# Performance work log

Hardware: AMD Instinct MI355X
Metric: run time of the kernel (lower is better)

The kernel has to match this reference:

```python
import jax, jax.numpy as jnp
import numpy as np

S, B, H = 2048, 32, 1024

def setup_inputs() -> dict:
    key = jax.random.key(0)
    ks = jax.random.split(key, 8)
    return {
        "hidden": jax.random.normal(ks[0], (1, B, H), dtype=jnp.float32),
        "hidden_sequence": jax.random.normal(ks[1], (S, B, H), dtype=jnp.float32),
        "input_masks": jax.random.bernoulli(ks[2], 0.5, (S, B)),
        "W1": jax.random.normal(ks[3], (H, H), dtype=jnp.float32) * 0.02,
        "b1": jax.random.normal(ks[4], (H,), dtype=jnp.float32) * 0.02,
        "W2": jax.random.normal(ks[5], (H, H), dtype=jnp.float32) * 0.02,
        "b2": jax.random.normal(ks[6], (H,), dtype=jnp.float32) * 0.02,
        "v": jax.random.uniform(ks[7], (H,), dtype=jnp.float32),
    }

def reference(hidden, hidden_sequence, input_masks, W1, b1, W2, b2, v):
    # hidden: (1,B,H) broadcast over S; hidden_sequence: (S,B,H)
    # additive (Bahdanau) energy: v . tanh(W1 hs + W2 h)  -> (S,B)
    pre = (jnp.einsum('sbh,kh->sbk', hidden_sequence, W1) + b1
           + jnp.einsum('obh,kh->obk', hidden, W2) + b2)  # (S,B,H)
    energy = jnp.einsum('sbh,h->sb', jnp.tanh(pre), v)     # (S,B)
    energy = jnp.where(input_masks, energy, jnp.float32(-1e10))
    attn = jax.nn.softmax(energy, axis=0)                  # softmax over seq per batch
    context = jnp.einsum('sb,sbh->bh', attn, hidden_sequence)[None]  # (1,B,H)
    return context
```

## Files before the change

### kernel.cpp

```cpp
#include <hip/hip_runtime.h>
#include <stdint.h>


#define SS 2048
#define BB 32
#define HH 1024
#define MM (SS*BB)

typedef _Float16 f16;
typedef __attribute__((ext_vector_type(8))) _Float16 f16x8;
typedef __attribute__((ext_vector_type(4))) _Float16 f16x4;
typedef __attribute__((ext_vector_type(4))) float   floatx4;

__device__ __forceinline__ float tanh_fast(float x) {
  float e = __expf(2.0f * x);
  return 1.0f - 2.0f / (e + 1.0f);
}

__device__ __forceinline__ void gload16(void* lds_base, const void* gptr) {
  __builtin_amdgcn_global_load_lds(
      (const __attribute__((address_space(1))) uint32_t*)(uintptr_t)gptr,
      (__attribute__((address_space(3))) uint32_t*)(uint32_t)(uintptr_t)lds_base,
      16, 0, 0);
}

#define BAR()   __builtin_amdgcn_s_barrier()
#define LGKM0() asm volatile("s_waitcnt lgkmcnt(0)" ::: "memory")
#define VMC4()  asm volatile("s_waitcnt vmcnt(4)" ::: "memory")
#define VMC0()  asm volatile("s_waitcnt vmcnt(0)" ::: "memory")

__global__ __launch_bounds__(256) void convert_f16(
    const float* __restrict__ hs, const float* __restrict__ W1,
    f16* __restrict__ hsf, f16* __restrict__ W1f)
{
  const size_t NH = (size_t)MM * HH;
  size_t base = ((size_t)blockIdx.x * 256 + threadIdx.x) * 8;
  if (base < NH) {
    floatx4 a = *(const floatx4*)&hs[base];
    floatx4 b = *(const floatx4*)&hs[base + 4];
    f16x8 o = {(f16)a.x,(f16)a.y,(f16)a.z,(f16)a.w,(f16)b.x,(f16)b.y,(f16)b.z,(f16)b.w};
    *(f16x8*)&hsf[base] = o;
  } else {
    size_t wb = base - NH;
    if (wb < (size_t)HH * HH) {
      floatx4 a = *(const floatx4*)&W1[wb];
      floatx4 b = *(const floatx4*)&W1[wb + 4];
      f16x8 o = {(f16)a.x,(f16)a.y,(f16)a.z,(f16)a.w,(f16)b.x,(f16)b.y,(f16)b.z,(f16)b.w};
      *(f16x8*)&W1f[wb] = o;
    }
  }
}

__global__ __launch_bounds__(256) void t2_kernel(
    const float* __restrict__ hidden, const float* __restrict__ W2,
    const float* __restrict__ b1, const float* __restrict__ b2,
    float* __restrict__ t2)
{
  const int gw   = blockIdx.x * 4 + (threadIdx.x >> 6);
  const int n    = gw >> 5;
  const int b    = gw & 31;
  const int lane = threadIdx.x & 63;
  float acc = 0.f;
#pragma unroll
  for (int q = 0; q < 4; ++q) {
    floatx4 hv = *(const floatx4*)&hidden[b * HH + q * 256 + lane * 4];
    floatx4 wv = *(const floatx4*)&W2[(size_t)n * HH + q * 256 + lane * 4];
    acc += hv.x * wv.x + hv.y * wv.y + hv.z * wv.z + hv.w * wv.w;
  }
#pragma unroll
  for (int off = 1; off < 64; off <<= 1) acc += __shfl_xor(acc, off);
  if (lane == 0) t2[b * HH + n] = acc + b1[n] + b2[n];
}

__global__ __launch_bounds__(512, 2) void gemm_energy_8p(
    const f16* __restrict__ hsf, const f16* __restrict__ W1f,
    const float* __restrict__ t2, const float* __restrict__ v,
    float* __restrict__ epart)
{
  __shared__ __align__(16) f16 Asm[2][2][128 * 64];
  __shared__ __align__(16) f16 Bsm[2][2][128 * 64];

  const int tid  = threadIdx.x;
  const int lane = tid & 63;
  const int w    = tid >> 6;
  const int quad = lane >> 4;
  const int l15  = lane & 15;
  const int wr   = w >> 2;
  const int wc   = w & 3;

  const int l  = blockIdx.x;
  const int x  = l & 7;
  const int j_ = l >> 3;
  const int nb = j_ & 3;
  const int mt = (j_ >> 2) * 8 + x;
  const int mB = mt * 256;
  const int nB = nb * 256;

  const int srow = w * 8 + (lane >> 3);
  const int sc0  = lane & 7;

  auto stA = [&](int buf, int half, int kt) {
#pragma unroll
    for (int q = 0; q < 2; ++q) {
      const int r  = q * 64 + srow;
      const int cb = sc0 ^ (r & 7);
      gload16(&Asm[buf][half][(q * 64 + w * 8) * 64],
              &hsf[(size_t)(mB + half * 128 + r) * HH + kt + cb * 8]);
    }
  };
  auto stB = [&](int buf, int half, int kt) {
#pragma unroll
    for (int q = 0; q < 2; ++q) {
      const int r  = q * 64 + srow;
      const int cb = sc0 ^ (r & 7);
      gload16(&Bsm[buf][half][(q * 64 + w * 8) * 64],
              &W1f[(size_t)(nB + half * 128 + r) * HH + kt + cb * 8]);
    }
  };

  floatx4 acc[8][4];
#pragma unroll
  for (int i = 0; i < 8; ++i)
#pragma unroll
    for (int j = 0; j < 4; ++j) acc[i][j] = (floatx4){0.f, 0.f, 0.f, 0.f};

  stB(0, 0, 0); stA(0, 0, 0); stA(0, 1, 0); stB(0, 1, 0);
  stB(1, 0, 64); stA(1, 0, 64);
  VMC4();
  BAR();

  f16x8 aF[2][4], b0F[2][2], b1F[2][2];
  const int bhalf  = wc >> 1;
  const int brbase = (wc & 1) * 64;

#pragma unroll 2
  for (int t = 0; t < 16; ++t) {
    const int buf = t & 1, nbuf = buf ^ 1;
    const int kt1 = (t + 1) * 64, kt2 = (t + 2) * 64;

#pragma unroll
    for (int ks = 0; ks < 2; ++ks) {
#pragma unroll
      for (int i = 0; i < 4; ++i) {
        const int rl = i * 16 + l15;
        const int cb = (ks * 4 + quad) ^ (rl & 7);
        aF[ks][i] = *(const f16x8*)&Asm[buf][wr][(rl * 8 + cb) * 8];
      }
#pragma unroll
      for (int j = 0; j < 2; ++j) {
        const int rl = brbase + j * 16 + l15;
        const int cb = (ks * 4 + quad) ^ (rl & 7);
        b0F[ks][j] = *(const f16x8*)&Bsm[buf][bhalf][(rl * 8 + cb) * 8];
      }
    }
    if (t < 15) stA(nbuf, 1, kt1);
    BAR(); LGKM0();
    __builtin_amdgcn_s_setprio(1);
#pragma unroll
    for (int ks = 0; ks < 2; ++ks)
#pragma unroll
      for (int i = 0; i < 4; ++i)
#pragma unroll
        for (int j = 0; j < 2; ++j)
          acc[i][j] = __builtin_amdgcn_mfma_f32_16x16x32_f16(aF[ks][i], b0F[ks][j], acc[i][j], 0, 0, 0);
    __builtin_amdgcn_s_setprio(0);
    BAR();

#pragma unroll
    for (int ks = 0; ks < 2; ++ks)
#pragma unroll
      for (int j = 0; j < 2; ++j) {
        const int rl = brbase + (j + 2) * 16 + l15;
        const int cb = (ks * 4 + quad) ^ (rl & 7);
        b1F[ks][j] = *(const f16x8*)&Bsm[buf][bhalf][(rl * 8 + cb) * 8];
      }
    if (t < 15) stB(nbuf, 1, kt1);
    BAR(); LGKM0();
    __builtin_amdgcn_s_setprio(1);
#pragma unroll
    for (int ks = 0; ks < 2; ++ks)
#pragma unroll
      for (int i = 0; i < 4; ++i)
#pragma unroll
        for (int j = 0; j < 2; ++j)
          acc[i][2 + j] = __builtin_amdgcn_mfma_f32_16x16x32_f16(aF[ks][i], b1F[ks][j], acc[i][2 + j], 0, 0, 0);
    __builtin_amdgcn_s_setprio(0);
    BAR();

#pragma unroll
    for (int ks = 0; ks < 2; ++ks)
#pragma unroll
      for (int i = 0; i < 4; ++i) {
        const int rl = 64 + i * 16 + l15;
        const int cb = (ks * 4 + quad) ^ (rl & 7);
        aF[ks][i] = *(const f16x8*)&Asm[buf][wr][(rl * 8 + cb) * 8];
      }
    if (t < 14) stB(buf, 0, kt2);
    BAR(); LGKM0();
    __builtin_amdgcn_s_setprio(1);
#pragma unroll
    for (int ks = 0; ks < 2; ++ks)
#pragma unroll
      for (int i = 0; i < 4; ++i)
#pragma unroll
        for (int j = 0; j < 2; ++j)
          acc[4 + i][2 + j] = __builtin_amdgcn_mfma_f32_16x16x32_f16(aF[ks][i], b1F[ks][j], acc[4 + i][2 + j], 0, 0, 0);
    __builtin_amdgcn_s_setprio(0);
    BAR();

    if (t < 14) stA(buf, 0, kt2);
    BAR();
    __builtin_amdgcn_s_setprio(1);
#pragma unroll
    for (int ks = 0; ks < 2; ++ks)
#pragma unroll
      for (int i = 0; i < 4; ++i)
#pragma unroll
        for (int j = 0; j < 2; ++j)
          acc[4 + i][j] = __builtin_amdgcn_mfma_f32_16x16x32_f16(aF[ks][i], b0F[ks][j], acc[4 + i][j], 0, 0, 0);
    __builtin_amdgcn_s_setprio(0);
    if (t < 14) { VMC4(); } else { VMC0(); }
    BAR();
  }

  float vv[4];
#pragma unroll
  for (int j = 0; j < 4; ++j) vv[j] = v[nB + wc * 64 + j * 16 + l15];
#pragma unroll
  for (int i = 0; i < 8; ++i) {
#pragma unroll
    for (int reg = 0; reg < 4; ++reg) {
      const int m = mB + wr * 128 + i * 16 + quad * 4 + reg;
      const int b = m & (BB - 1);
      const int s = m >> 5;
      float rs = 0.f;
#pragma unroll
      for (int j = 0; j < 4; ++j) {
        const int n = nB + wc * 64 + j * 16 + l15;
        rs += tanh_fast(acc[i][j][reg] + t2[b * HH + n]) * vv[j];
      }
      rs += __shfl_xor(rs, 1);
      rs += __shfl_xor(rs, 2);
      rs += __shfl_xor(rs, 4);
      rs += __shfl_xor(rs, 8);
      if (l15 == 0) epart[(size_t)(nb * 4 + wc) * MM + b * SS + s] = rs;
    }
  }
}

__global__ __launch_bounds__(1024) void softmax16t(
    const float* __restrict__ epart, const int* __restrict__ masks,
    float* __restrict__ attn)
{
  const int b = blockIdx.x;
  const int tid = threadIdx.x;
  __shared__ float redm[16], reds[16];
  float em[2];
  float lmax = -3e38f;
#pragma unroll
  for (int it = 0; it < 2; ++it) {
    const int s = it * 1024 + tid;
    float e = 0.f;
#pragma unroll
    for (int p = 0; p < 16; ++p) e += epart[(size_t)p * MM + b * SS + s];
    if (masks[s * BB + b] == 0) e = -1e10f;
    em[it] = e;
    lmax = fmaxf(lmax, e);
  }
#pragma unroll
  for (int off = 1; off < 64; off <<= 1) lmax = fmaxf(lmax, __shfl_xor(lmax, off));
  if ((tid & 63) == 0) redm[tid >> 6] = lmax;
  __syncthreads();
#pragma unroll
  for (int i = 0; i < 16; ++i) lmax = fmaxf(lmax, redm[i]);
  float lsum = 0.f;
#pragma unroll
  for (int it = 0; it < 2; ++it) { em[it] = __expf(em[it] - lmax); lsum += em[it]; }
#pragma unroll
  for (int off = 1; off < 64; off <<= 1) lsum += __shfl_xor(lsum, off);
  if ((tid & 63) == 0) reds[tid >> 6] = lsum;
  __syncthreads();
  float tsum = 0.f;
#pragma unroll
  for (int i = 0; i < 16; ++i) tsum += reds[i];
  const float inv = 1.0f / tsum;
#pragma unroll
  for (int it = 0; it < 2; ++it) attn[b * SS + it * 1024 + tid] = em[it] * inv;
}

__global__ __launch_bounds__(256) void context_f16t(
    const f16* __restrict__ hsf, const float* __restrict__ attn,
    float* __restrict__ ctxp)
{
  const int b  = blockIdx.x;
  const int sc = blockIdx.y;
  const int tid = threadIdx.x;
  __shared__ float sat[64];
  if (tid < 64) sat[tid] = attn[b * SS + sc * 64 + tid];
  __syncthreads();
  floatx4 acc = {0.f, 0.f, 0.f, 0.f};
#pragma unroll 4
  for (int s = 0; s < 64; ++s) {
    const float a = sat[s];
    if (a != 0.f) {
      f16x4 h = *(const f16x4*)&hsf[(size_t)((sc * 64 + s) * BB + b) * HH + tid * 4];
      acc.x += a * (float)h[0];
      acc.y += a * (float)h[1];
      acc.z += a * (float)h[2];
      acc.w += a * (float)h[3];
    }
  }
  *(floatx4*)&ctxp[(size_t)(sc * BB + b) * HH + tid * 4] = acc;
}

__global__ __launch_bounds__(256) void ctx_reduce32(
    const float* __restrict__ ctxp, float* __restrict__ out)
{
  const int i = blockIdx.x * 256 + threadIdx.x;
  float s = 0.f;
#pragma unroll
  for (int sc = 0; sc < 32; ++sc) s += ctxp[(size_t)sc * (BB * HH) + i];
  out[i] = s;
}

__global__ __launch_bounds__(256) void gemm_energy_fb(
    const float* __restrict__ hs, const float* __restrict__ W1,
    const float* __restrict__ t2, const float* __restrict__ v,
    float* __restrict__ epart)
{
  const int tid = threadIdx.x;
  const int nb  = blockIdx.x;
  const int mB  = blockIdx.y * 128;
  __shared__ __align__(16) f16 Asm[128][72];
  __shared__ __align__(16) f16 Bsm[128][72];
  const int lane = tid & 63;
  const int w    = tid >> 6;
  const int quad = lane >> 4;
  const int l15  = lane & 15;
  floatx4 acc[2][8];
#pragma unroll
  for (int i = 0; i < 2; ++i)
#pragma unroll
    for (int j = 0; j < 8; ++j) acc[i][j] = (floatx4){0.f, 0.f, 0.f, 0.f};
  const int srow = tid >> 4;
  const int scol = (tid & 15) * 4;
  const float* Abase = hs + (size_t)(mB + srow) * HH + scol;
  const float* Bbase = W1 + (size_t)(nb * 128 + srow) * HH + scol;
  for (int kt = 0; kt < HH; kt += 64) {
#pragma unroll
    for (int p = 0; p < 8; ++p) {
      floatx4 fa = *(const floatx4*)(Abase + (size_t)(p * 16) * HH + kt);
      floatx4 fb = *(const floatx4*)(Bbase + (size_t)(p * 16) * HH + kt);
      f16x4 ha = {(f16)fa.x, (f16)fa.y, (f16)fa.z, (f16)fa.w};
      f16x4 hb = {(f16)fb.x, (f16)fb.y, (f16)fb.z, (f16)fb.w};
      *(f16x4*)&Asm[p * 16 + srow][scol] = ha;
      *(f16x4*)&Bsm[p * 16 + srow][scol] = hb;
    }
    __syncthreads();
#pragma unroll
    for (int ks = 0; ks < 2; ++ks) {
      f16x8 af[2], bfr[8];
#pragma unroll
      for (int i = 0; i < 2; ++i)
        af[i] = *(const f16x8*)&Asm[w * 32 + i * 16 + l15][ks * 32 + quad * 8];
#pragma unroll
      for (int j = 0; j < 8; ++j)
        bfr[j] = *(const f16x8*)&Bsm[j * 16 + l15][ks * 32 + quad * 8];
#pragma unroll
      for (int i = 0; i < 2; ++i)
#pragma unroll
        for (int j = 0; j < 8; ++j)
          acc[i][j] = __builtin_amdgcn_mfma_f32_16x16x32_f16(af[i], bfr[j], acc[i][j], 0, 0, 0);
    }
    __syncthreads();
  }
  const int nB = nb * 128;
#pragma unroll
  for (int i = 0; i < 2; ++i) {
#pragma unroll
    for (int reg = 0; reg < 4; ++reg) {
      const int m = mB + w * 32 + i * 16 + quad * 4 + reg;
      const int b = m & (BB - 1);
      float rs = 0.f;
#pragma unroll
      for (int j = 0; j < 8; ++j) {
        const int n = nB + j * 16 + l15;
        rs += tanh_fast(acc[i][j][reg] + t2[b * HH + n]) * v[n];
      }
      rs += __shfl_xor(rs, 1);
      rs += __shfl_xor(rs, 2);
      rs += __shfl_xor(rs, 4);
      rs += __shfl_xor(rs, 8);
      if (l15 == 0) epart[(size_t)nb * MM + m] = rs;
    }
  }
}

__global__ __launch_bounds__(256) void softmax8(
    const float* __restrict__ epart, const int* __restrict__ masks,
    float* __restrict__ attn)
{
  const int b = blockIdx.x;
  const int tid = threadIdx.x;
  __shared__ float redm[4], reds[4];
  float em[8];
  float lmax = -3e38f;
#pragma unroll
  for (int it = 0; it < 8; ++it) {
    const int s = it * 256 + tid;
    float e = 0.f;
#pragma unroll
    for (int p = 0; p < 8; ++p) e += epart[(size_t)p * MM + s * BB + b];
    if (masks[s * BB + b] == 0) e = -1e10f;
    em[it] = e;
    lmax = fmaxf(lmax, e);
  }
#pragma unroll
  for (int off = 1; off < 64; off <<= 1) lmax = fmaxf(lmax, __shfl_xor(lmax, off));
  if ((tid & 63) == 0) redm[tid >> 6] = lmax;
  __syncthreads();
  lmax = fmaxf(fmaxf(redm[0], redm[1]), fmaxf(redm[2], redm[3]));
  float lsum = 0.f;
#pragma unroll
  for (int it = 0; it < 8; ++it) { em[it] = __expf(em[it] - lmax); lsum += em[it]; }
#pragma unroll
  for (int off = 1; off < 64; off <<= 1) lsum += __shfl_xor(lsum, off);
  if ((tid & 63) == 0) reds[tid >> 6] = lsum;
  __syncthreads();
  const float inv = 1.0f / (reds[0] + reds[1] + reds[2] + reds[3]);
#pragma unroll
  for (int it = 0; it < 8; ++it) attn[(it * 256 + tid) * BB + b] = em[it] * inv;
}

__global__ __launch_bounds__(256) void context_fb(
    const float* __restrict__ hs, const float* __restrict__ attn,
    float* __restrict__ ctxp)
{
  const int b  = blockIdx.x;
  const int sc = blockIdx.y;
  const int tid = threadIdx.x;
  floatx4 acc = {0.f, 0.f, 0.f, 0.f};
  for (int s = sc * 256; s < sc * 256 + 256; ++s) {
    const float a = attn[s * BB + b];
    if (a != 0.f) {
      floatx4 h = *(const floatx4*)&hs[(size_t)(s * BB + b) * HH + tid * 4];
      acc.x += a * h.x; acc.y += a * h.y; acc.z += a * h.z; acc.w += a * h.w;
    }
  }
  *(floatx4*)&ctxp[(size_t)(sc * BB + b) * HH + tid * 4] = acc;
}

__global__ __launch_bounds__(256) void ctx_reduce8(
    const float* __restrict__ ctxp, float* __restrict__ out)
{
  const int i = blockIdx.x * 256 + threadIdx.x;
  float s = 0.f;
#pragma unroll
  for (int sc = 0; sc < 8; ++sc) s += ctxp[(size_t)sc * (BB * HH) + i];
  out[i] = s;
}

extern "C" void kernel_launch(void* const* d_in, const int* in_sizes, int n_in,
                              void* d_out, int out_size, void* d_ws, size_t ws_size,
                              hipStream_t stream) {
  const float* hidden = (const float*)d_in[0];
  const float* hs     = (const float*)d_in[1];
  const int*   masks  = (const int*)d_in[2];
  const float* W1     = (const float*)d_in[3];
  const float* b1     = (const float*)d_in[4];
  const float* W2     = (const float*)d_in[5];
  const float* b2     = (const float*)d_in[6];
  const float* v      = (const float*)d_in[7];
  float* out = (float*)d_out;

  const size_t hsf_b   = (size_t)MM * HH * 2;
  const size_t w1f_b   = (size_t)HH * HH * 2;
  const size_t epart_b = (size_t)16 * MM * 4;
  const size_t attn_b  = (size_t)MM * 4;
  const size_t t2_b    = (size_t)BB * HH * 4;
  const size_t ctxp_b  = (size_t)32 * BB * HH * 4;
  const size_t need = hsf_b + w1f_b + epart_b + attn_b + t2_b + ctxp_b;

  if (ws_size >= need) {
    char* p = (char*)d_ws;
    f16*   hsf   = (f16*)p;              p += hsf_b;
    f16*   W1f   = (f16*)p;              p += w1f_b;
    float* epart = (float*)p;            p += epart_b;
    float* attn  = (float*)p;            p += attn_b;
    float* t2    = (float*)p;            p += t2_b;
    float* ctxp  = (float*)p;

    convert_f16<<<dim3(33280), 256, 0, stream>>>(hs, W1, hsf, W1f);
    t2_kernel<<<dim3(BB * HH / 4), 256, 0, stream>>>(hidden, W2, b1, b2, t2);
    gemm_energy_8p<<<dim3(1024), 512, 0, stream>>>(hsf, W1f, t2, v, epart);
    softmax16t<<<dim3(BB), 1024, 0, stream>>>(epart, masks, attn);
    context_f16t<<<dim3(BB, 32), 256, 0, stream>>>(hsf, attn, ctxp);
    ctx_reduce32<<<dim3(BB * HH / 256), 256, 0, stream>>>(ctxp, out);
  } else {
    float* epart = (float*)d_ws;
    float* attn  = epart + 8 * MM;
    float* t2    = attn + MM;
    float* ctxp  = t2 + BB * HH;

    t2_kernel<<<dim3(BB * HH / 4), 256, 0, stream>>>(hidden, W2, b1, b2, t2);
    gemm_energy_fb<<<dim3(8, MM / 128), 256, 0, stream>>>(hs, W1, t2, v, epart);
    softmax8<<<dim3(BB), 256, 0, stream>>>(epart, masks, attn);
    context_fb<<<dim3(BB, 8), 256, 0, stream>>>(hs, attn, ctxp);
    ctx_reduce8<<<dim3(BB * HH / 256), 256, 0, stream>>>(ctxp, out);
  }
}
```

Before: 575.3 us.

## Drop intra-iteration GEMM barriers, fuse prep kernels, stage t2 in LDS, DPP reduce

Removes several barrier plus lgkmcnt(0) waits between the async global-to-LDS loads and the MFMA phases of the main GEMM loop. The loop now relies on the end-of-iteration vmcnt wait and barrier for ordering, which cuts stalls but could race if any LDS buffer reuse depended on the removed barriers. It also merges the f16 conversion and the t2 projection into one launch, and changes the conversion access pattern. In the epilogue, the t2 tile is staged in LDS and the 16-lane shuffle reduction is replaced with DPP row operations.

```diff
diff --git a/kernel.cpp b/kernel.cpp
--- a/kernel.cpp
+++ b/kernel.cpp
@@ -25,51 +25,58 @@
 }
 
 #define BAR()   __builtin_amdgcn_s_barrier()
-#define LGKM0() asm volatile("s_waitcnt lgkmcnt(0)" ::: "memory")
 #define VMC4()  asm volatile("s_waitcnt vmcnt(4)" ::: "memory")
 #define VMC0()  asm volatile("s_waitcnt vmcnt(0)" ::: "memory")
 
-__global__ __launch_bounds__(256) void convert_f16(
+__device__ __forceinline__ float dpp_red16(float x) {
+  int t;
+  t = __builtin_amdgcn_update_dpp(0, __float_as_int(x), 0xB1, 0xF, 0xF, true);
+  x += __int_as_float(t);
+  t = __builtin_amdgcn_update_dpp(0, __float_as_int(x), 0x4E, 0xF, 0xF, true);
+  x += __int_as_float(t);
+  t = __builtin_amdgcn_update_dpp(0, __float_as_int(x), 0x141, 0xF, 0xF, true);
+  x += __int_as_float(t);
+  t = __builtin_amdgcn_update_dpp(0, __float_as_int(x), 0x140, 0xF, 0xF, true);
+  x += __int_as_float(t);
+  return x;
+}
+
+__global__ __launch_bounds__(256) void prep_kernel(
     const float* __restrict__ hs, const float* __restrict__ W1,
-    f16* __restrict__ hsf, f16* __restrict__ W1f)
-{
-  const size_t NH = (size_t)MM * HH;
-  size_t base = ((size_t)blockIdx.x * 256 + threadIdx.x) * 8;
-  if (base < NH) {
-    floatx4 a = *(const floatx4*)&hs[base];
-    floatx4 b = *(const floatx4*)&hs[base + 4];
-    f16x8 o = {(f16)a.x,(f16)a.y,(f16)a.z,(f16)a.w,(f16)b.x,(f16)b.y,(f16)b.z,(f16)b.w};
-    *(f16x8*)&hsf[base] = o;
-  } else {
-    size_t wb = base - NH;
-    if (wb < (size_t)HH * HH) {
-      floatx4 a = *(const floatx4*)&W1[wb];
-      floatx4 b = *(const floatx4*)&W1[wb + 4];
-      f16x8 o = {(f16)a.x,(f16)a.y,(f16)a.z,(f16)a.w,(f16)b.x,(f16)b.y,(f16)b.z,(f16)b.w};
-      *(f16x8*)&W1f[wb] = o;
-    }
-  }
-}
-
-__global__ __launch_bounds__(256) void t2_kernel(
     const float* __restrict__ hidden, const float* __restrict__ W2,
     const float* __restrict__ b1, const float* __restrict__ b2,
-    float* __restrict__ t2)
-{
-  const int gw   = blockIdx.x * 4 + (threadIdx.x >> 6);
-  const int n    = gw >> 5;
-  const int b    = gw & 31;
-  const int lane = threadIdx.x & 63;
-  float acc = 0.f;
-#pragma unroll
-  for (int q = 0; q < 4; ++q) {
-    floatx4 hv = *(const floatx4*)&hidden[b * HH + q * 256 + lane * 4];
-    floatx4 wv = *(const floatx4*)&W2[(size_t)n * HH + q * 256 + lane * 4];
-    acc += hv.x * wv.x + hv.y * wv.y + hv.z * wv.z + hv.w * wv.w;
-  }
-#pragma unroll
-  for (int off = 1; off < 64; off <<= 1) acc += __shfl_xor(acc, off);
-  if (lane == 0) t2[b * HH + n] = acc + b1[n] + b2[n];
+    f16* __restrict__ hsf, f16* __restrict__ W1f, float* __restrict__ t2)
+{
+  const int bid = blockIdx.x;
+  if (bid < 33280) {
+    const size_t NH = (size_t)MM * HH;
+    size_t g0 = (size_t)bid * 2048 + threadIdx.x * 4;
+    const float* src;
+    f16* dst;
+    if (g0 < NH) { src = hs; dst = hsf; }
+    else         { src = W1 - NH; dst = W1f - NH; }
+    floatx4 a = *(const floatx4*)&src[g0];
+    floatx4 b = *(const floatx4*)&src[g0 + 1024];
+    f16x4 oa = {(f16)a.x,(f16)a.y,(f16)a.z,(f16)a.w};
+    f16x4 ob = {(f16)b.x,(f16)b.y,(f16)b.z,(f16)b.w};
+    *(f16x4*)&dst[g0] = oa;
+    *(f16x4*)&dst[g0 + 1024] = ob;
+  } else {
+    const int gw   = (bid - 33280) * 4 + (threadIdx.x >> 6);
+    const int n    = gw >> 5;
+    const int b    = gw & 31;
+    const int lane = threadIdx.x & 63;
+    float acc = 0.f;
+#pragma unroll
+    for (int q = 0; q < 4; ++q) {
+      floatx4 hv = *(const floatx4*)&hidden[b * HH + q * 256 + lane * 4];
+      floatx4 wv = *(const floatx4*)&W2[(size_t)n * HH + q * 256 + lane * 4];
+      acc += hv.x * wv.x + hv.y * wv.y + hv.z * wv.z + hv.w * wv.w;
+    }
+#pragma unroll
+    for (int off = 1; off < 64; off <<= 1) acc += __shfl_xor(acc, off);
+    if (lane == 0) t2[b * HH + n] = acc + b1[n] + b2[n];
+  }
 }
 
 __global__ __launch_bounds__(512, 2) void gemm_energy_8p(
@@ -154,7 +161,6 @@
       }
     }
     if (t < 15) stA(nbuf, 1, kt1);
-    BAR(); LGKM0();
     __builtin_amdgcn_s_setprio(1);
 #pragma unroll
     for (int ks = 0; ks < 2; ++ks)
@@ -175,7 +181,6 @@
         b1F[ks][j] = *(const f16x8*)&Bsm[buf][bhalf][(rl * 8 + cb) * 8];
       }
     if (t < 15) stB(nbuf, 1, kt1);
-    BAR(); LGKM0();
     __builtin_amdgcn_s_setprio(1);
 #pragma unroll
     for (int ks = 0; ks < 2; ++ks)
@@ -196,7 +201,6 @@
         aF[ks][i] = *(const f16x8*)&Asm[buf][wr][(rl * 8 + cb) * 8];
       }
     if (t < 14) stB(buf, 0, kt2);
-    BAR(); LGKM0();
     __builtin_amdgcn_s_setprio(1);
 #pragma unroll
     for (int ks = 0; ks < 2; ++ks)
@@ -209,7 +213,6 @@
     BAR();
 
     if (t < 14) stA(buf, 0, kt2);
-    BAR();
     __builtin_amdgcn_s_setprio(1);
 #pragma unroll
     for (int ks = 0; ks < 2; ++ks)
@@ -223,6 +226,18 @@
     BAR();
   }
 
+  float* t2s = (float*)&Asm[0][0][0];
+  {
+    const int r = tid >> 4;
+    const int c = (tid & 15) * 16;
+#pragma unroll
+    for (int q = 0; q < 4; ++q) {
+      floatx4 tv = *(const floatx4*)&t2[r * HH + nB + c + q * 4];
+      *(floatx4*)&t2s[r * 257 + c + q * 4] = tv;
+    }
+  }
+  __syncthreads();
+
   float vv[4];
 #pragma unroll
   for (int j = 0; j < 4; ++j) vv[j] = v[nB + wc * 64 + j * 16 + l15];
@@ -236,13 +251,10 @@
       float rs = 0.f;
 #pragma unroll
       for (int j = 0; j < 4; ++j) {
-        const int n = nB + wc * 64 + j * 16 + l15;
-        rs += tanh_fast(acc[i][j][reg] + t2[b * HH + n]) * vv[j];
+        const int n = wc * 64 + j * 16 + l15;
+        rs += tanh_fast(acc[i][j][reg] + t2s[b * 257 + n]) * vv[j];
       }
-      rs += __shfl_xor(rs, 1);
-      rs += __shfl_xor(rs, 2);
-      rs += __shfl_xor(rs, 4);
-      rs += __shfl_xor(rs, 8);
+      rs = dpp_red16(rs);
       if (l15 == 0) epart[(size_t)(nb * 4 + wc) * MM + b * SS + s] = rs;
     }
   }
@@ -323,6 +335,27 @@
   out[i] = s;
 }
 
+__global__ __launch_bounds__(256) void t2_kernel(
+    const float* __restrict__ hidden, const float* __restrict__ W2,
+    const float* __restrict__ b1, const float* __restrict__ b2,
+    float* __restrict__ t2)
+{
+  const int gw   = blockIdx.x * 4 + (threadIdx.x >> 6);
+  const int n    = gw >> 5;
+  const int b    = gw & 31;
+  const int lane = threadIdx.x & 63;
+  float acc = 0.f;
+#pragma unroll
+  for (int q = 0; q < 4; ++q) {
+    floatx4 hv = *(const floatx4*)&hidden[b * HH + q * 256 + lane * 4];
+    floatx4 wv = *(const floatx4*)&W2[(size_t)n * HH + q * 256 + lane * 4];
+    acc += hv.x * wv.x + hv.y * wv.y + hv.z * wv.z + hv.w * wv.w;
+  }
+#pragma unroll
+  for (int off = 1; off < 64; off <<= 1) acc += __shfl_xor(acc, off);
+  if (lane == 0) t2[b * HH + n] = acc + b1[n] + b2[n];
+}
+
 __global__ __launch_bounds__(256) void gemm_energy_fb(
     const float* __restrict__ hs, const float* __restrict__ W1,
     const float* __restrict__ t2, const float* __restrict__ v,
@@ -490,8 +523,7 @@
     float* t2    = (float*)p;            p += t2_b;
     float* ctxp  = (float*)p;
 
-    convert_f16<<<dim3(33280), 256, 0, stream>>>(hs, W1, hsf, W1f);
-    t2_kernel<<<dim3(BB * HH / 4), 256, 0, stream>>>(hidden, W2, b1, b2, t2);
+    prep_kernel<<<dim3(33280 + 8192), 256, 0, stream>>>(hs, W1, hidden, W2, b1, b2, hsf, W1f, t2);
     gemm_energy_8p<<<dim3(1024), 512, 0, stream>>>(hsf, W1f, t2, v, epart);
     softmax16t<<<dim3(BB), 1024, 0, stream>>>(epart, masks, attn);
     context_f16t<<<dim3(BB, 32), 256, 0, stream>>>(hsf, attn, ctxp);
```

After: 569.5 us. No clear change (-1.0%).
